# Kernel tuning notes

Hardware: AMD Instinct MI355X
Metric: run time of the kernel (lower is better)

The kernel has to match this reference:

```python
import jax, jax.numpy as jnp
import numpy as np
from jax import lax

B, N, D = 16, 2048, 256
H = 64  # hidden_dim
EPS = 1e-5


def zero_softmax(x, eps=EPS):
    # zeros stay exactly zero: exp(0)-1 == 0
    e = jnp.exp(x) - 1.0
    return e / (jnp.sum(e, axis=-1, keepdims=True) + eps)


def setup_inputs() -> dict:
    key = jax.random.key(0)
    ks = jax.random.split(key, 9)
    s_in = 1.0 / np.sqrt(D)
    x = jax.random.normal(ks[0], (B, N, D), dtype=jnp.float32)
    Wq = jax.random.uniform(ks[1], (D, H), jnp.float32, -s_in, s_in)
    bq = jax.random.uniform(ks[2], (H,), jnp.float32, -s_in, s_in)
    Wk = jax.random.uniform(ks[3], (D, H), jnp.float32, -s_in, s_in)
    bk = jax.random.uniform(ks[4], (H,), jnp.float32, -s_in, s_in)
    Wv = jax.random.uniform(ks[5], (D, H), jnp.float32, -s_in, s_in)
    bv = jax.random.uniform(ks[6], (H,), jnp.float32, -s_in, s_in)
    s_c = 1.0 / 3.0  # conv fan_in = 1*3*3 = 9
    conv_w = jax.random.uniform(ks[7], (1, 1, 3, 3), jnp.float32, -s_c, s_c)
    conv_b = jax.random.uniform(ks[8], (1,), jnp.float32, -s_c, s_c)
    return {"x": x, "Wq": Wq, "bq": bq, "Wk": Wk, "bk": bk,
            "Wv": Wv, "bv": bv, "conv_w": conv_w, "conv_b": conv_b}


def reference(x, Wq, bq, Wk, bk, Wv, bv, conv_w, conv_b):
    scale = H ** (-0.5)
    q = jnp.einsum('bnd,dh->bnh', x, Wq) + bq
    k = jnp.einsum('bnd,dh->bnh', x, Wk) + bk
    v = jnp.einsum('bnd,dh->bnh', x, Wv) + bv
    A_dense = jnp.einsum('bnh,bmh->bnm', q, k) * scale  # [B, N, N]
    A_in = A_dense[:, None, :, :]  # [B, 1, N, N]
    A_conv = lax.conv_general_dilated(
        A_in, conv_w, window_strides=(1, 1), padding='SAME',
        dimension_numbers=('NCHW', 'OIHW', 'NCHW')) + conv_b[None, :, None, None]
    A_conv = jax.nn.sigmoid(A_conv)[:, 0, :, :]
    A_sparse = jax.nn.relu(A_dense - A_conv)
    A_norm = zero_softmax(A_sparse)
    return jnp.einsum('bnm,bmh->bnh', A_norm, v)
```

## Files before the change

kernel.cpp:

```cpp
#include <hip/hip_runtime.h>
#include <hip/hip_bf16.h>

typedef __bf16 bf16_t;
typedef __bf16 bf16x8 __attribute__((ext_vector_type(8)));
typedef float  floatx4 __attribute__((ext_vector_type(4)));

#define BQ 16
#define NTOK 2048
#define DIM 256
#define HD 64

__global__ __launch_bounds__(256) void k_prep(const float* __restrict__ Wq,
                                              const float* __restrict__ Wk,
                                              const float* __restrict__ Wv,
                                              bf16_t* __restrict__ wt,
                                              float* __restrict__ outz,
                                              float* __restrict__ rsz) {
    int o = blockIdx.x * 256 + threadIdx.x;
    if (o < 49152) {
        int w = o >> 14;
        int r = o & 16383;
        int h = r >> 8;
        int d = r & 255;
        const float* W = (w == 0) ? Wq : ((w == 1) ? Wk : Wv);
        wt[o] = (bf16_t)W[d * 64 + h];
    }
    float4 z = make_float4(0.f, 0.f, 0.f, 0.f);
    for (int u = o; u < 532480; u += 262144) {
        if (u < 524288) ((float4*)outz)[u] = z;
        else            ((float4*)rsz)[u - 524288] = z;
    }
}

#define XS 264
__global__ __launch_bounds__(256) void k_qkv(const float* __restrict__ x,
                                             const bf16_t* __restrict__ wt,
                                             const float* __restrict__ bq,
                                             const float* __restrict__ bk,
                                             const float* __restrict__ bv,
                                             bf16_t* __restrict__ qb,
                                             bf16_t* __restrict__ kb,
                                             bf16_t* __restrict__ vt) {
    __shared__ bf16_t x_ls[64 * XS];
    __shared__ bf16_t vt_ls[64 * 72];

    int b  = blockIdx.x >> 5;
    int t0 = (blockIdx.x & 31) << 6;
    int t  = threadIdx.x;
    int lane = t & 63;
    int w    = t >> 6;
    int m_   = lane & 15;
    int q4   = lane >> 4;

    for (int tau = t; tau < 4096; tau += 256) {
        int row = tau >> 6, ch = tau & 63;
        float4 v = ((const float4*)x)[(size_t)(b * NTOK + t0 + row) * 64 + ch];
        bf16_t tmp[4] = {(bf16_t)v.x, (bf16_t)v.y, (bf16_t)v.z, (bf16_t)v.w};
        *(uint2*)(&x_ls[row * XS + ch * 4]) = *(uint2*)tmp;
    }
    __syncthreads();

    for (int wi = 0; wi < 3; ++wi) {
        const bf16_t* wtw = wt + wi * 16384;
        floatx4 acc[4];
        #pragma unroll
        for (int mt = 0; mt < 4; ++mt) acc[mt] = floatx4{0.f, 0.f, 0.f, 0.f};

        #pragma unroll
        for (int ks = 0; ks < 8; ++ks) {
            bf16x8 bfrag = *(const bf16x8*)(wtw + (16 * w + m_) * 256 + ks * 32 + q4 * 8);
            #pragma unroll
            for (int mt = 0; mt < 4; ++mt) {
                bf16x8 afrag = *(const bf16x8*)(&x_ls[(16 * mt + m_) * XS + ks * 32 + q4 * 8]);
                acc[mt] = __builtin_amdgcn_mfma_f32_16x16x32_bf16(afrag, bfrag, acc[mt], 0, 0, 0);
            }
        }
        const float* bias_p = (wi == 0) ? bq : ((wi == 1) ? bk : bv);
        float bias = bias_p[16 * w + m_];
        float scale = (wi == 0) ? 0.125f : 1.0f;

        if (wi < 2) {
            bf16_t* dst = (wi == 0) ? qb : kb;
            #pragma unroll
            for (int mt = 0; mt < 4; ++mt)
                #pragma unroll
                for (int r = 0; r < 4; ++r) {
                    int tok = t0 + 16 * mt + 4 * q4 + r;
                    dst[(size_t)(b * NTOK + tok) * 64 + 16 * w + m_] = (bf16_t)((acc[mt][r] + bias) * scale);
                }
        } else {
            #pragma unroll
            for (int mt = 0; mt < 4; ++mt)
                #pragma unroll
                for (int r = 0; r < 4; ++r)
                    vt_ls[(16 * w + m_) * 72 + 16 * mt + 4 * q4 + r] = (bf16_t)(acc[mt][r] + bias);
            __syncthreads();
            for (int tau = t; tau < 512; tau += 256) {
                int h = tau >> 3, ch = tau & 7;
                uint4 val = *(const uint4*)(&vt_ls[h * 72 + ch * 8]);
                *(uint4*)(vt + (size_t)(b * 64 + h) * NTOK + t0 + ch * 8) = val;
            }
        }
    }
}

#define SA 52
#define SP 72
#define RINT 46
#define NIT_C 15
__global__ __launch_bounds__(256) void k_attn(const bf16_t* __restrict__ qb,
                                              const bf16_t* __restrict__ kb,
                                              const bf16_t* __restrict__ vt,
                                              const float* __restrict__ conv_w,
                                              const float* __restrict__ conv_b,
                                              float* __restrict__ outp,
                                              float* __restrict__ rsg) {
    __shared__ bf16_t q_ls[48 * SP];
    __shared__ bf16_t k_ls[48 * SP];
    __shared__ bf16_t v_ls[64 * SP];
    __shared__ float  A_ls[48 * SA];
    __shared__ bf16_t p_ls[48 * SP];

    int b    = blockIdx.z;
    int r0   = blockIdx.x * RINT;
    int ch0  = blockIdx.y * NIT_C;
    int t = threadIdx.x, lane = t & 63, w = t >> 6;
    int m_ = lane & 15, q4 = lane >> 4;

    const uint* vt32 = (const uint*)vt + (size_t)b * 64 * 1024;

    int vh[6], vc[6];
    #pragma unroll
    for (int j = 0; j < 6; ++j) { int tau = t + 256 * j; vh[j] = tau / 23; vc[j] = tau % 23; }

    float cw[9];
    #pragma unroll
    for (int i = 0; i < 9; ++i) cw[i] = conv_w[i];
    float cb = conv_b[0];

    uint4 kreg[2];
    uint  vreg[6];
    auto prefetch = [&](int c0) {
        {
            int row = t >> 3, ch = t & 7;
            int g = c0 - 1 + row;
            uint4 val = make_uint4(0u, 0u, 0u, 0u);
            if (g >= 0 && g < NTOK)
                val = *(const uint4*)(kb + (size_t)(b * NTOK + g) * 64 + ch * 8);
            kreg[0] = val;
        }
        if (t < 128) {
            int row = (t + 256) >> 3, ch = t & 7;
            int g = c0 - 1 + row;
            uint4 val = make_uint4(0u, 0u, 0u, 0u);
            if (g >= 0 && g < NTOK)
                val = *(const uint4*)(kb + (size_t)(b * NTOK + g) * 64 + ch * 8);
            kreg[1] = val;
        }
        #pragma unroll
        for (int j = 0; j < 6; ++j) {
            if (t + 256 * j < 1472) {
                int n = c0 + 2 * vc[j];
                uint val = 0u;
                if (n < NTOK) val = vt32[vh[j] * 1024 + (n >> 1)];
                vreg[j] = val;
            }
        }
    };

    prefetch(ch0 * RINT);

    for (int u = t; u < 1728; u += 256) ((uint*)p_ls)[u] = 0u;
    for (int u = t; u < 1152; u += 256) {
        int h = u / 18, c = 46 + u % 18;
        v_ls[h * SP + c] = (bf16_t)0.f;
    }
    if (t < 192) A_ls[(t >> 2) * SA + 48 + (t & 3)] = 0.f;
    for (int tau = t; tau < 384; tau += 256) {
        int row = tau >> 3, ch = tau & 7;
        int g = r0 - 1 + row;
        uint4 val = make_uint4(0u, 0u, 0u, 0u);
        if (g >= 0 && g < NTOK)
            val = *(const uint4*)(qb + (size_t)(b * NTOK + g) * 64 + ch * 8);
        *(uint4*)(&q_ls[row * SP + ch * 8]) = val;
    }

    floatx4 accO[3];
    #pragma unroll
    for (int ti = 0; ti < 3; ++ti) accO[ti] = floatx4{0.f, 0.f, 0.f, 0.f};
    float rs[3] = {0.f, 0.f, 0.f};

    for (int it = 0; it < NIT_C; ++it) {
        {
            int row = t >> 3, ch = t & 7;
            *(uint4*)(&k_ls[row * SP + ch * 8]) = kreg[0];
            if (t < 128) {
                int row1 = (t + 256) >> 3;
                *(uint4*)(&k_ls[row1 * SP + ch * 8]) = kreg[1];
            }
            #pragma unroll
            for (int j = 0; j < 6; ++j)
                if (t + 256 * j < 1472)
                    *(uint*)(&v_ls[vh[j] * SP + 2 * vc[j]]) = vreg[j];
        }
        __syncthreads();

        for (int T = w; T < 9; T += 4) {
            int ti = T / 3, tj = T % 3;
            floatx4 a = floatx4{0.f, 0.f, 0.f, 0.f};
            #pragma unroll
            for (int ks = 0; ks < 2; ++ks) {
                bf16x8 af = *(const bf16x8*)(&q_ls[(16 * ti + m_) * SP + ks * 32 + q4 * 8]);
                bf16x8 bf = *(const bf16x8*)(&k_ls[(16 * tj + m_) * SP + ks * 32 + q4 * 8]);
                a = __builtin_amdgcn_mfma_f32_16x16x32_bf16(af, bf, a, 0, 0, 0);
            }
            #pragma unroll
            for (int r = 0; r < 4; ++r)
                A_ls[(16 * ti + 4 * q4 + r) * SA + 16 * tj + m_] = a[r];
        }
        __syncthreads();

        if (it + 1 < NIT_C) prefetch((ch0 + it + 1) * RINT);

        #pragma unroll
        for (int round = 0; round < 3; ++round) {
            int idx = t + (round << 8);
            if (idx < 552) {
                int i = idx / 12 + 1;
                int g = idx - (i - 1) * 12;
                const float* base = &A_ls[(i - 1) * SA + 4 * g];
                float a0[6], a1[6], a2[6];
                *(float4*)(a0) = *(const float4*)(base);
                *(float2*)(a0 + 4) = *(const float2*)(base + 4);
                *(float4*)(a1) = *(const float4*)(base + SA);
                *(float2*)(a1 + 4) = *(const float2*)(base + SA + 4);
                *(float4*)(a2) = *(const float4*)(base + 2 * SA);
                *(float2*)(a2 + 4) = *(const float2*)(base + 2 * SA + 4);
                float esum = 0.f;
                bf16_t quad[4];
                #pragma unroll
                for (int x = 0; x < 4; ++x) {
                    float conv = cb
                        + cw[0] * a0[x] + cw[1] * a0[x + 1] + cw[2] * a0[x + 2]
                        + cw[3] * a1[x] + cw[4] * a1[x + 1] + cw[5] * a1[x + 2]
                        + cw[6] * a2[x] + cw[7] * a2[x + 1] + cw[8] * a2[x + 2];
                    float sig = __builtin_amdgcn_rcpf(1.f + __expf(-conv));
                    float s = fmaxf(a1[x + 1] - sig, 0.f);
                    float ev = __expf(s) - 1.f;
                    if (4 * g + x > 45) ev = 0.f;
                    quad[x] = (bf16_t)ev;
                    esum += ev;
                }
                rs[round] += esum;
                *(uint2*)(&p_ls[i * SP + 4 * g]) = *(uint2*)quad;
            }
        }
        __syncthreads();

        #pragma unroll
        for (int ks = 0; ks < 2; ++ks) {
            bf16x8 bf = *(const bf16x8*)(&v_ls[(16 * w + m_) * SP + ks * 32 + q4 * 8]);
            #pragma unroll
            for (int ti = 0; ti < 3; ++ti) {
                bf16x8 af = *(const bf16x8*)(&p_ls[(16 * ti + m_) * SP + ks * 32 + q4 * 8]);
                accO[ti] = __builtin_amdgcn_mfma_f32_16x16x32_bf16(af, bf, accO[ti], 0, 0, 0);
            }
        }
        __syncthreads();
    }

    float* sc = A_ls;
    sc[t * 3 + 0] = rs[0];
    sc[t * 3 + 1] = rs[1];
    sc[t * 3 + 2] = rs[2];
    __syncthreads();
    if (t < RINT) {
        float s = 0.f;
        #pragma unroll
        for (int j = 0; j < 12; ++j) {
            int idx = 12 * t + j;
            s += sc[(idx & 255) * 3 + (idx >> 8)];
        }
        int grow = r0 + t;
        if (grow < NTOK) atomicAdd(&rsg[b * NTOK + grow], s);
    }

    #pragma unroll
    for (int ti = 0; ti < 3; ++ti) {
        #pragma unroll
        for (int r = 0; r < 4; ++r) {
            int i = 16 * ti + 4 * q4 + r;
            int grow = r0 + i - 1;
            if (i >= 1 && i < 47 && grow < NTOK)
                atomicAdd(&outp[((size_t)(b * NTOK + grow) << 6) + 16 * w + m_], accO[ti][r]);
        }
    }
}

__global__ __launch_bounds__(256) void k_norm(float* __restrict__ out,
                                              const float* __restrict__ rsg) {
    int gid = blockIdx.x * 256 + threadIdx.x;
    float4 o = ((float4*)out)[gid];
    float d = rsg[gid >> 4] + 1e-5f;
    float inv = 1.f / d;
    o.x *= inv; o.y *= inv; o.z *= inv; o.w *= inv;
    ((float4*)out)[gid] = o;
}

extern "C" void kernel_launch(void* const* d_in, const int* in_sizes, int n_in,
                              void* d_out, int out_size, void* d_ws, size_t ws_size,
                              hipStream_t stream) {
    const float* x  = (const float*)d_in[0];
    const float* Wq = (const float*)d_in[1];
    const float* bq = (const float*)d_in[2];
    const float* Wk = (const float*)d_in[3];
    const float* bk = (const float*)d_in[4];
    const float* Wv = (const float*)d_in[5];
    const float* bv = (const float*)d_in[6];
    const float* cw = (const float*)d_in[7];
    const float* cb = (const float*)d_in[8];
    float* out = (float*)d_out;

    char* ws = (char*)d_ws;
    bf16_t* wt = (bf16_t*)ws;
    bf16_t* qb = (bf16_t*)(ws + 98304);
    bf16_t* kb = (bf16_t*)(ws + 98304 + 4194304);
    bf16_t* vt = (bf16_t*)(ws + 98304 + 8388608);
    float*  rsg = (float*)(ws + 98304 + 12582912);

    k_prep<<<dim3(1024), dim3(256), 0, stream>>>(Wq, Wk, Wv, wt, out, rsg);
    k_qkv<<<dim3(512), dim3(256), 0, stream>>>(x, wt, bq, bk, bv, qb, kb, vt);
    k_attn<<<dim3(45, 3, BQ), dim3(256), 0, stream>>>(qb, kb, vt, cw, cb, out, rsg);
    k_norm<<<dim3(2048), dim3(256), 0, stream>>>(out, rsg);
}
```

Baseline: 226.5 us.

## Enlarge attention tile to 64x64 with 512 threads and register-resident Q

The attention kernel now works on 64x64 tiles (62 interior rows/cols) with 8 waves per block instead of 48x48 with 4 waves. Each wave keeps its Q fragments in registers instead of shared memory, and the column chunks are split unevenly across 4 y-blocks. The exponentials are rewritten as exp2 with log2e folded into the conv weights, the column mask becomes a multiply, and row sums are reduced with shuffles instead of a shared-memory pass. Larger tiles cut the halo-recompute overhead and the number of atomics per output, at the cost of more shared memory and registers per block and fewer blocks in the grid.

```diff
diff --git a/kernel.cpp b/kernel.cpp
--- a/kernel.cpp
+++ b/kernel.cpp
@@ -104,42 +104,45 @@
     }
 }
 
-#define SA 52
+#define SA 68
 #define SP 72
-#define RINT 46
-#define NIT_C 15
-__global__ __launch_bounds__(256) void k_attn(const bf16_t* __restrict__ qb,
-                                              const bf16_t* __restrict__ kb,
-                                              const bf16_t* __restrict__ vt,
-                                              const float* __restrict__ conv_w,
-                                              const float* __restrict__ conv_b,
-                                              float* __restrict__ outp,
-                                              float* __restrict__ rsg) {
-    __shared__ bf16_t q_ls[48 * SP];
-    __shared__ bf16_t k_ls[48 * SP];
+#define RINT 62
+#define L2E 1.44269504f
+
+static __device__ __forceinline__ bf16x8 as_bf16x8(uint4 u) {
+    union { uint4 a; bf16x8 b; } c; c.a = u; return c.b;
+}
+
+__global__ __launch_bounds__(512, 6) void k_attn(const bf16_t* __restrict__ qb,
+                                                 const bf16_t* __restrict__ kb,
+                                                 const bf16_t* __restrict__ vt,
+                                                 const float* __restrict__ conv_w,
+                                                 const float* __restrict__ conv_b,
+                                                 float* __restrict__ outp,
+                                                 float* __restrict__ rsg) {
+    __shared__ bf16_t k_ls[64 * SP];
     __shared__ bf16_t v_ls[64 * SP];
-    __shared__ float  A_ls[48 * SA];
-    __shared__ bf16_t p_ls[48 * SP];
-
-    int b    = blockIdx.z;
-    int r0   = blockIdx.x * RINT;
-    int ch0  = blockIdx.y * NIT_C;
+    __shared__ bf16_t p_ls[64 * SP];
+    __shared__ float  A_ls[64 * SA];
+
+    int b  = blockIdx.z;
+    int r0 = blockIdx.x * RINT;
+    int it_beg = (int)(blockIdx.y * 34) >> 2;
+    int it_end = (int)((blockIdx.y + 1) * 34) >> 2;
+
     int t = threadIdx.x, lane = t & 63, w = t >> 6;
     int m_ = lane & 15, q4 = lane >> 4;
+    int wtj = w & 3;
+    int wti = (w >> 2) << 1;
 
     const uint* vt32 = (const uint*)vt + (size_t)b * 64 * 1024;
 
-    int vh[6], vc[6];
-    #pragma unroll
-    for (int j = 0; j < 6; ++j) { int tau = t + 256 * j; vh[j] = tau / 23; vc[j] = tau % 23; }
-
-    float cw[9];
-    #pragma unroll
-    for (int i = 0; i < 9; ++i) cw[i] = conv_w[i];
-    float cb = conv_b[0];
-
-    uint4 kreg[2];
-    uint  vreg[6];
+    int vh[4], vc[4];
+    #pragma unroll
+    for (int j = 0; j < 4; ++j) { int tau = t + 512 * j; vh[j] = tau / 31; vc[j] = tau % 31; }
+
+    uint4 kreg;
+    uint  vreg[4];
     auto prefetch = [&](int c0) {
         {
             int row = t >> 3, ch = t & 7;
@@ -147,19 +150,11 @@
             uint4 val = make_uint4(0u, 0u, 0u, 0u);
             if (g >= 0 && g < NTOK)
                 val = *(const uint4*)(kb + (size_t)(b * NTOK + g) * 64 + ch * 8);
-            kreg[0] = val;
-        }
-        if (t < 128) {
-            int row = (t + 256) >> 3, ch = t & 7;
-            int g = c0 - 1 + row;
-            uint4 val = make_uint4(0u, 0u, 0u, 0u);
-            if (g >= 0 && g < NTOK)
-                val = *(const uint4*)(kb + (size_t)(b * NTOK + g) * 64 + ch * 8);
-            kreg[1] = val;
-        }
-        #pragma unroll
-        for (int j = 0; j < 6; ++j) {
-            if (t + 256 * j < 1472) {
+            kreg = val;
+        }
+        #pragma unroll
+        for (int j = 0; j < 4; ++j) {
+            if (t + 512 * j < 1984) {
                 int n = c0 + 2 * vc[j];
                 uint val = 0u;
                 if (n < NTOK) val = vt32[vh[j] * 1024 + (n >> 1)];
@@ -168,73 +163,84 @@
         }
     };
 
-    prefetch(ch0 * RINT);
-
-    for (int u = t; u < 1728; u += 256) ((uint*)p_ls)[u] = 0u;
-    for (int u = t; u < 1152; u += 256) {
-        int h = u / 18, c = 46 + u % 18;
-        v_ls[h * SP + c] = (bf16_t)0.f;
-    }
-    if (t < 192) A_ls[(t >> 2) * SA + 48 + (t & 3)] = 0.f;
-    for (int tau = t; tau < 384; tau += 256) {
-        int row = tau >> 3, ch = tau & 7;
-        int g = r0 - 1 + row;
-        uint4 val = make_uint4(0u, 0u, 0u, 0u);
-        if (g >= 0 && g < NTOK)
-            val = *(const uint4*)(qb + (size_t)(b * NTOK + g) * 64 + ch * 8);
-        *(uint4*)(&q_ls[row * SP + ch * 8]) = val;
-    }
-
-    floatx4 accO[3];
-    #pragma unroll
-    for (int ti = 0; ti < 3; ++ti) accO[ti] = floatx4{0.f, 0.f, 0.f, 0.f};
-    float rs[3] = {0.f, 0.f, 0.f};
-
-    for (int it = 0; it < NIT_C; ++it) {
+    prefetch(it_beg * RINT);
+
+    float cw[9];
+    #pragma unroll
+    for (int i = 0; i < 9; ++i) cw[i] = conv_w[i] * L2E;
+    float cb = conv_b[0] * L2E;
+
+    float msk[4];
+    #pragma unroll
+    for (int x = 0; x < 4; ++x) msk[x] = (4 * (t & 15) + x <= 61) ? 1.f : 0.f;
+
+    bf16x8 qreg[2][2];
+    #pragma unroll
+    for (int p = 0; p < 2; ++p) {
+        int g = r0 - 1 + 16 * (wti + p) + m_;
+        #pragma unroll
+        for (int ks = 0; ks < 2; ++ks) {
+            uint4 val = make_uint4(0u, 0u, 0u, 0u);
+            if (g >= 0 && g < NTOK)
+                val = *(const uint4*)(qb + (size_t)(b * NTOK + g) * 64 + ks * 32 + q4 * 8);
+            qreg[p][ks] = as_bf16x8(val);
+        }
+    }
+
+    for (int u = t; u < 2304; u += 512) ((uint*)p_ls)[u] = 0u;
+    if (t < 320) {
+        int h = t / 5, c = 62 + 2 * (t % 5);
+        *(uint*)(&v_ls[h * SP + c]) = 0u;
+    }
+    if (t < 256) A_ls[(t >> 2) * SA + 64 + (t & 3)] = 0.f;
+
+    floatx4 accO[2];
+    accO[0] = floatx4{0.f, 0.f, 0.f, 0.f};
+    accO[1] = floatx4{0.f, 0.f, 0.f, 0.f};
+    float rs[2] = {0.f, 0.f};
+
+    int i0 = (t >> 4) + 1;
+    int gq = t & 15;
+    int cvoff = (i0 - 1) * SA + 4 * gq;
+
+    for (int itg = it_beg; itg < it_end; ++itg) {
         {
             int row = t >> 3, ch = t & 7;
-            *(uint4*)(&k_ls[row * SP + ch * 8]) = kreg[0];
-            if (t < 128) {
-                int row1 = (t + 256) >> 3;
-                *(uint4*)(&k_ls[row1 * SP + ch * 8]) = kreg[1];
-            }
-            #pragma unroll
-            for (int j = 0; j < 6; ++j)
-                if (t + 256 * j < 1472)
+            *(uint4*)(&k_ls[row * SP + ch * 8]) = kreg;
+            #pragma unroll
+            for (int j = 0; j < 4; ++j)
+                if (t + 512 * j < 1984)
                     *(uint*)(&v_ls[vh[j] * SP + 2 * vc[j]]) = vreg[j];
         }
         __syncthreads();
 
-        for (int T = w; T < 9; T += 4) {
-            int ti = T / 3, tj = T % 3;
+        #pragma unroll
+        for (int p = 0; p < 2; ++p) {
             floatx4 a = floatx4{0.f, 0.f, 0.f, 0.f};
             #pragma unroll
             for (int ks = 0; ks < 2; ++ks) {
-                bf16x8 af = *(const bf16x8*)(&q_ls[(16 * ti + m_) * SP + ks * 32 + q4 * 8]);
-                bf16x8 bf = *(const bf16x8*)(&k_ls[(16 * tj + m_) * SP + ks * 32 + q4 * 8]);
-                a = __builtin_amdgcn_mfma_f32_16x16x32_bf16(af, bf, a, 0, 0, 0);
-            }
+                bf16x8 bfr = *(const bf16x8*)(&k_ls[(16 * wtj + m_) * SP + ks * 32 + q4 * 8]);
+                a = __builtin_amdgcn_mfma_f32_16x16x32_bf16(qreg[p][ks], bfr, a, 0, 0, 0);
+            }
+            int rbase = 16 * (wti + p) + 4 * q4;
             #pragma unroll
             for (int r = 0; r < 4; ++r)
-                A_ls[(16 * ti + 4 * q4 + r) * SA + 16 * tj + m_] = a[r];
+                A_ls[(rbase + r) * SA + 16 * wtj + m_] = a[r];
         }
         __syncthreads();
 
-        if (it + 1 < NIT_C) prefetch((ch0 + it + 1) * RINT);
-
-        #pragma unroll
-        for (int round = 0; round < 3; ++round) {
-            int idx = t + (round << 8);
-            if (idx < 552) {
-                int i = idx / 12 + 1;
-                int g = idx - (i - 1) * 12;
-                const float* base = &A_ls[(i - 1) * SA + 4 * g];
+        if (itg + 1 < it_end) prefetch((itg + 1) * RINT);
+
+        #pragma unroll
+        for (int round = 0; round < 2; ++round) {
+            if (round == 0 || t < 480) {
+                const float* base = &A_ls[cvoff + round * (32 * SA)];
                 float a0[6], a1[6], a2[6];
-                *(float4*)(a0) = *(const float4*)(base);
+                *(float4*)(a0)     = *(const float4*)(base);
                 *(float2*)(a0 + 4) = *(const float2*)(base + 4);
-                *(float4*)(a1) = *(const float4*)(base + SA);
+                *(float4*)(a1)     = *(const float4*)(base + SA);
                 *(float2*)(a1 + 4) = *(const float2*)(base + SA + 4);
-                *(float4*)(a2) = *(const float4*)(base + 2 * SA);
+                *(float4*)(a2)     = *(const float4*)(base + 2 * SA);
                 *(float2*)(a2 + 4) = *(const float2*)(base + 2 * SA + 4);
                 float esum = 0.f;
                 bf16_t quad[4];
@@ -244,55 +250,51 @@
                         + cw[0] * a0[x] + cw[1] * a0[x + 1] + cw[2] * a0[x + 2]
                         + cw[3] * a1[x] + cw[4] * a1[x + 1] + cw[5] * a1[x + 2]
                         + cw[6] * a2[x] + cw[7] * a2[x + 1] + cw[8] * a2[x + 2];
-                    float sig = __builtin_amdgcn_rcpf(1.f + __expf(-conv));
+                    float sig = __builtin_amdgcn_rcpf(1.f + __builtin_amdgcn_exp2f(-conv));
                     float s = fmaxf(a1[x + 1] - sig, 0.f);
-                    float ev = __expf(s) - 1.f;
-                    if (4 * g + x > 45) ev = 0.f;
+                    float ev = (__builtin_amdgcn_exp2f(s * L2E) - 1.f) * msk[x];
                     quad[x] = (bf16_t)ev;
                     esum += ev;
                 }
                 rs[round] += esum;
-                *(uint2*)(&p_ls[i * SP + 4 * g]) = *(uint2*)quad;
+                *(uint2*)(&p_ls[(i0 + round * 32) * SP + 4 * gq]) = *(uint2*)quad;
             }
         }
         __syncthreads();
 
         #pragma unroll
         for (int ks = 0; ks < 2; ++ks) {
-            bf16x8 bf = *(const bf16x8*)(&v_ls[(16 * w + m_) * SP + ks * 32 + q4 * 8]);
-            #pragma unroll
-            for (int ti = 0; ti < 3; ++ti) {
-                bf16x8 af = *(const bf16x8*)(&p_ls[(16 * ti + m_) * SP + ks * 32 + q4 * 8]);
-                accO[ti] = __builtin_amdgcn_mfma_f32_16x16x32_bf16(af, bf, accO[ti], 0, 0, 0);
+            bf16x8 bfr = *(const bf16x8*)(&v_ls[(16 * wtj + m_) * SP + ks * 32 + q4 * 8]);
+            #pragma unroll
+            for (int p = 0; p < 2; ++p) {
+                bf16x8 af = *(const bf16x8*)(&p_ls[(16 * (wti + p) + m_) * SP + ks * 32 + q4 * 8]);
+                accO[p] = __builtin_amdgcn_mfma_f32_16x16x32_bf16(af, bfr, accO[p], 0, 0, 0);
             }
         }
         __syncthreads();
     }
 
-    float* sc = A_ls;
-    sc[t * 3 + 0] = rs[0];
-    sc[t * 3 + 1] = rs[1];
-    sc[t * 3 + 2] = rs[2];
-    __syncthreads();
-    if (t < RINT) {
-        float s = 0.f;
-        #pragma unroll
-        for (int j = 0; j < 12; ++j) {
-            int idx = 12 * t + j;
-            s += sc[(idx & 255) * 3 + (idx >> 8)];
-        }
-        int grow = r0 + t;
-        if (grow < NTOK) atomicAdd(&rsg[b * NTOK + grow], s);
-    }
-
-    #pragma unroll
-    for (int ti = 0; ti < 3; ++ti) {
+    float s0 = rs[0], s1 = rs[1];
+    #pragma unroll
+    for (int d = 1; d < 16; d <<= 1) {
+        s0 += __shfl_xor(s0, d);
+        s1 += __shfl_xor(s1, d);
+    }
+    if ((t & 15) == 0) {
+        int g0 = r0 + i0 - 1;
+        if (g0 < NTOK) atomicAdd(&rsg[b * NTOK + g0], s0);
+        if (t < 480 && g0 + 32 < NTOK) atomicAdd(&rsg[b * NTOK + g0 + 32], s1);
+    }
+
+    #pragma unroll
+    for (int p = 0; p < 2; ++p) {
+        int rbase = 16 * (wti + p) + 4 * q4;
         #pragma unroll
         for (int r = 0; r < 4; ++r) {
-            int i = 16 * ti + 4 * q4 + r;
+            int i = rbase + r;
             int grow = r0 + i - 1;
-            if (i >= 1 && i < 47 && grow < NTOK)
-                atomicAdd(&outp[((size_t)(b * NTOK + grow) << 6) + 16 * w + m_], accO[ti][r]);
+            if (i >= 1 && i < 63 && grow < NTOK)
+                atomicAdd(&outp[((size_t)(b * NTOK + grow) << 6) + 16 * wtj + m_], accO[p][r]);
         }
     }
 }
@@ -330,6 +332,6 @@
 
     k_prep<<<dim3(1024), dim3(256), 0, stream>>>(Wq, Wk, Wv, wt, out, rsg);
     k_qkv<<<dim3(512), dim3(256), 0, stream>>>(x, wt, bq, bk, bv, qb, kb, vt);
-    k_attn<<<dim3(45, 3, BQ), dim3(256), 0, stream>>>(qb, kb, vt, cw, cb, out, rsg);
+    k_attn<<<dim3(34, 4, BQ), dim3(512), 0, stream>>>(qb, kb, vt, cw, cb, out, rsg);
     k_norm<<<dim3(2048), dim3(256), 0, stream>>>(out, rsg);
 }
```

Result: slower. 277.6 us (+22.6%).
